# Optimization experiments

Measured on AMD Instinct MI355X. Metric: run time of the kernel, lower is better.

The kernel has to match this reference:

```python
import jax, jax.numpy as jnp
import numpy as np

HEAD_DIM = 64
NUM_Q_HEADS = 32
NUM_KV_HEADS = 8
ROPE_FREQ = 10000.0
EPS = 1e-6


def _rms_norm(x, gamma):
    # normalize over last dim (head_dim)
    var = jnp.mean(jnp.square(x), axis=-1, keepdims=True)
    return x * jax.lax.rsqrt(var + EPS) * gamma


def _rope_cos_sin(seq_len, dtype=jnp.float32):
    inv_freq = 1.0 / (ROPE_FREQ ** (jnp.arange(0, HEAD_DIM, 2, dtype=jnp.float32) / HEAD_DIM))
    pos = jnp.arange(seq_len, dtype=jnp.float32)
    freqs = pos[:, None] * inv_freq[None, :]          # [S, hd/2]
    emb = jnp.concatenate([freqs, freqs], axis=-1)    # [S, hd]
    return jnp.cos(emb).astype(dtype), jnp.sin(emb).astype(dtype)


def _rotate_half(x):
    x1, x2 = jnp.split(x, 2, axis=-1)
    return jnp.concatenate([-x2, x1], axis=-1)


def _apply_rope(x, cos, sin):
    # x: [B, H, S, hd]; cos/sin: [S, hd]
    return x * cos[None, None, :, :] + _rotate_half(x) * sin[None, None, :, :]


def setup_inputs() -> dict:
    key = jax.random.key(0)
    ks = jax.random.split(key, 5)
    B, S, D = 2, 2048, 2048
    qkv_out = (NUM_Q_HEADS + 2 * NUM_KV_HEADS) * HEAD_DIM  # 3072
    x = jax.random.normal(ks[0], (B, S, D), dtype=jnp.float32)
    w_qkv = jax.random.normal(ks[1], (qkv_out, D), dtype=jnp.float32) * (D ** -0.5)
    w_out = jax.random.normal(ks[2], (D, NUM_Q_HEADS * HEAD_DIM), dtype=jnp.float32) * ((NUM_Q_HEADS * HEAD_DIM) ** -0.5)
    q_gamma = jnp.ones((HEAD_DIM,), dtype=jnp.float32)
    k_gamma = jnp.ones((HEAD_DIM,), dtype=jnp.float32)
    return {"x": x, "w_qkv": w_qkv, "w_out": w_out, "q_gamma": q_gamma, "k_gamma": k_gamma}


def reference(x, w_qkv, w_out, q_gamma, k_gamma):
    B, S, D = x.shape
    groups = NUM_Q_HEADS // NUM_KV_HEADS
    # fused QKV projection (no bias)
    qkv = jnp.einsum("bsd,od->bso", x, w_qkv)
    qkv = qkv.reshape(B, S, NUM_Q_HEADS + 2 * NUM_KV_HEADS, HEAD_DIM)
    qkv = jnp.transpose(qkv, (0, 2, 1, 3))  # [B, heads, S, hd]
    q = qkv[:, :NUM_Q_HEADS]
    k = qkv[:, NUM_Q_HEADS:NUM_Q_HEADS + NUM_KV_HEADS]
    v = qkv[:, NUM_Q_HEADS + NUM_KV_HEADS:]
    # QK RMSNorm over head_dim
    q = _rms_norm(q, q_gamma)
    k = _rms_norm(k, k_gamma)
    # RoPE
    cos, sin = _rope_cos_sin(S, dtype=x.dtype)
    q = _apply_rope(q, cos, sin)
    k = _apply_rope(k, cos, sin)
    # GQA: repeat-interleave kv heads
    k = jnp.repeat(k, groups, axis=1)
    v = jnp.repeat(v, groups, axis=1)
    # causal SDPA
    scale = HEAD_DIM ** -0.5
    scores = jnp.einsum("bhqd,bhkd->bhqk", q, k) * scale
    causal = jnp.tril(jnp.ones((S, S), dtype=bool))
    scores = jnp.where(causal[None, None], scores, jnp.finfo(scores.dtype).min)
    attn = jax.nn.softmax(scores, axis=-1)
    ctx = jnp.einsum("bhqk,bhkd->bhqd", attn, v)
    ctx = jnp.transpose(ctx, (0, 2, 1, 3)).reshape(B, S, NUM_Q_HEADS * HEAD_DIM)
    out = jnp.einsum("bsf,df->bsd", ctx, w_out)
    return out
```

## Files before the change

### kernel.cpp

```cpp
#include <hip/hip_runtime.h>

typedef _Float16 f16;
typedef __fp16 fp16x2 __attribute__((ext_vector_type(2)));
typedef _Float16 f16x8 __attribute__((ext_vector_type(8)));
typedef float f32x4 __attribute__((ext_vector_type(4)));
typedef float f32x16 __attribute__((ext_vector_type(16)));

#define AS1 __attribute__((address_space(1)))
#define AS3 __attribute__((address_space(3)))

#define SCALE_L2E 0.18033688011112042f


__device__ __forceinline__ void gload16(const void* g, void* l) {
    __builtin_amdgcn_global_load_lds(
        (const AS1 unsigned*)(unsigned long long)g,
        (AS3 unsigned*)(unsigned)(unsigned long long)l,
        16, 0, 0);
}

__device__ __forceinline__ unsigned pk2(float a, float b) {
    union { fp16x2 v; unsigned u; } c;
    c.v = __builtin_amdgcn_cvt_pkrtz(a, b);
    return c.u;
}

#define BAR() do { asm volatile("" ::: "memory"); __builtin_amdgcn_s_barrier(); asm volatile("" ::: "memory"); } while (0)


__global__ __launch_bounds__(256) void k_cast_all(const float* __restrict__ x,
                                                  const float* __restrict__ wq,
                                                  const float* __restrict__ wo,
                                                  f16* __restrict__ Xh,
                                                  f16* __restrict__ Wqh,
                                                  f16* __restrict__ Woh,
                                                  float* __restrict__ cosT,
                                                  float* __restrict__ sinT) {
    if (blockIdx.x >= 18432) {
        int idx = (blockIdx.x - 18432) * 256 + threadIdx.x;
        int s = idx >> 5, i = idx & 31;
        float ang = (float)s * exp2f(-(float)i * 0.4152410118609190f);
        cosT[idx] = cosf(ang);
        sinT[idx] = sinf(ang);
        return;
    }
    int i = (blockIdx.x * 256 + threadIdx.x) * 4;
    const float* src; f16* dst;
    if (i < 8388608)        { src = x  + i;            dst = Xh  + i; }
    else if (i < 14680064)  { src = wq + (i - 8388608); dst = Wqh + (i - 8388608); }
    else                    { src = wo + (i - 14680064); dst = Woh + (i - 14680064); }
    float4 v = *(const float4*)src;
    union { f16 h[4]; ushort4 u; } c;
    c.h[0] = (f16)v.x; c.h[1] = (f16)v.y; c.h[2] = (f16)v.z; c.h[3] = (f16)v.w;
    *(ushort4*)dst = c.u;
}


template <typename OutT, int NU>
__global__ __launch_bounds__(512, 2) void k_gemm256(const f16* __restrict__ A,
                                                    const f16* __restrict__ Bt,
                                                    OutT* __restrict__ C,
                                                    int M, int N, int K) {
    constexpr int BUFSZ = 32768 + NU * 8192;
    __shared__ __align__(16) char sm[2 * BUFSZ];
    const int tid = threadIdx.x;
    const int lane = tid & 63, wid = tid >> 6;
    const int wm = wid >> 2, wn = wid & 3;
    const int lr = lane & 15, g4 = lane >> 4;

    const int gx = gridDim.x;
    const int nwg = gx * gridDim.y;
    int lin = blockIdx.y * gx + blockIdx.x;
    lin = (lin & 7) * (nwg >> 3) + (lin >> 3);
    const int bx = lin % gx, by = lin / gx;
    const int m0 = by * 256, n0 = bx * (64 * NU);
    const int NT = K >> 6;

    const int srow = tid >> 3;
    const int scol = ((tid & 7) ^ (srow & 7)) * 8;
    const f16* gA = A  + (size_t)(m0 + srow) * K + scol;
    const f16* gB = Bt + (size_t)(n0 + srow) * K + scol;

    auto STGA = [&](int t, int h) {
        char* d = sm + (t & 1) * BUFSZ + h * 16384 + tid * 16;
        gload16(gA + (size_t)(h * 128) * K + t * 64,      d);
        gload16(gA + (size_t)(h * 128 + 64) * K + t * 64, d + 8192);
    };
    auto STGB = [&](int t) {
#pragma unroll
        for (int u = 0; u < NU; u++)
            gload16(gB + (size_t)(u * 64) * K + t * 64,
                    sm + (t & 1) * BUFSZ + 32768 + u * 8192 + tid * 16);
    };

    f32x4 acc[8][NU] = {};
    f16x8 bfr[NU];

    STGA(0, 0); STGA(0, 1); STGB(0);
    STGA(1, 0); STGA(1, 1); STGB(1);
    if constexpr (NU == 2) asm volatile("s_waitcnt vmcnt(6)" ::: "memory");
    else                   asm volatile("s_waitcnt vmcnt(7)" ::: "memory");
    BAR();

    for (int t = 0; t < NT; ++t) {
        const int buf = t & 1;
        const char* bA = sm + buf * BUFSZ + wm * 16384;
        const char* bB = sm + buf * BUFSZ + 32768;
        const bool sA = (t >= 1) && (t + 1 < NT);
        const bool sB = (t + 2 < NT);
#pragma unroll
        for (int p = 0; p < 4; ++p) {
            const int kk = p >> 1, mh = p & 1;
            f16x8 afr[4];
            if (mh == 0) {
#pragma unroll
                for (int n = 0; n < NU; n++) {
                    const int r = wn * (16 * NU) + n * 16 + lr;
                    bfr[n] = *(const f16x8*)(bB + ((r * 128 + kk * 64 + g4 * 16) ^ ((r & 7) << 4)));
                }
            }
#pragma unroll
            for (int i = 0; i < 4; i++) {
                const int r = (mh * 4 + i) * 16 + lr;
                afr[i] = *(const f16x8*)(bA + ((r * 128 + kk * 64 + g4 * 16) ^ ((r & 7) << 4)));
            }
            if (p == 0 && sA) STGA(t + 1, 0);
            if (p == 1 && sA) STGA(t + 1, 1);
            if (p == 3 && sB) STGB(t + 2);
            BAR();
            asm volatile("s_waitcnt lgkmcnt(0)" ::: "memory");
            __builtin_amdgcn_s_setprio(1);
#pragma unroll
            for (int i = 0; i < 4; i++)
#pragma unroll
                for (int n = 0; n < NU; n++)
                    acc[mh * 4 + i][n] = __builtin_amdgcn_mfma_f32_16x16x32_f16(afr[i], bfr[n], acc[mh * 4 + i][n], 0, 0, 0);
            __builtin_amdgcn_s_setprio(0);
            if (p == 3 && t + 1 < NT) {
                if (t + 2 < NT) {
                    if constexpr (NU == 2) asm volatile("s_waitcnt vmcnt(2)" ::: "memory");
                    else                   asm volatile("s_waitcnt vmcnt(3)" ::: "memory");
                } else {
                    asm volatile("s_waitcnt vmcnt(0)" ::: "memory");
                }
            }
            BAR();
        }
    }

#pragma unroll
    for (int m = 0; m < 8; m++)
#pragma unroll
        for (int n = 0; n < NU; n++) {
            size_t base = (size_t)(m0 + wm * 128 + m * 16 + g4 * 4) * N + (n0 + wn * (16 * NU) + n * 16 + lr);
#pragma unroll
            for (int j = 0; j < 4; j++)
                C[base + (size_t)j * N] = (OutT)acc[m][n][j];
        }
}


__global__ __launch_bounds__(256) void k_qkv_post(const f16* __restrict__ qkv,
                                                  const float* __restrict__ qg,
                                                  const float* __restrict__ kg,
                                                  const float* __restrict__ cosT,
                                                  const float* __restrict__ sinT,
                                                  f16* __restrict__ Qf,
                                                  f16* __restrict__ Kf,
                                                  f16* __restrict__ Vf) {
    __shared__ f16 tl[4][8][72];
    const int tid = threadIdx.x, lane = tid & 63, wv = tid >> 6;
    const int gw = blockIdx.x * 4 + wv;
    const int b = gw / 12288;
    const int r0 = gw - b * 12288;
    const int head = r0 >> 8;
    const int sblk = r0 & 255;
    const int s0 = sblk * 8;
    const int s_loc = lane >> 3, ch = lane & 7;
    const int s = s0 + s_loc;

    f16x8 v = *(const f16x8*)&qkv[((size_t)b * 2048 + s) * 3072 + head * 64 + ch * 8];

    if (head < 40) {
        float vf[8];
#pragma unroll
        for (int j = 0; j < 8; j++) vf[j] = (float)v[j];
        float ss = 0.f;
#pragma unroll
        for (int j = 0; j < 8; j++) ss += vf[j] * vf[j];
        ss += __shfl_xor(ss, 1); ss += __shfl_xor(ss, 2); ss += __shfl_xor(ss, 4);
        float rinv = rsqrtf(ss * (1.0f / 64.0f) + 1e-6f);
        const float* gam = (head < 32 ? qg : kg) + ch * 8;
        float4 g0 = *(const float4*)gam, g1 = *(const float4*)(gam + 4);
        float gv[8] = {g0.x, g0.y, g0.z, g0.w, g1.x, g1.y, g1.z, g1.w};
        float xn[8], ot[8];
#pragma unroll
        for (int j = 0; j < 8; j++) xn[j] = vf[j] * rinv * gv[j];
#pragma unroll
        for (int j = 0; j < 8; j++) ot[j] = __shfl_xor(xn[j], 4);
        const int i0 = (ch & 3) * 8;
        float4 c0  = *(const float4*)&cosT[(s << 5) + i0];
        float4 c1  = *(const float4*)&cosT[(s << 5) + i0 + 4];
        float4 sn0 = *(const float4*)&sinT[(s << 5) + i0];
        float4 sn1 = *(const float4*)&sinT[(s << 5) + i0 + 4];
        float cs[8] = {c0.x, c0.y, c0.z, c0.w, c1.x, c1.y, c1.z, c1.w};
        float sn[8] = {sn0.x, sn0.y, sn0.z, sn0.w, sn1.x, sn1.y, sn1.z, sn1.w};
        float sgn = (ch < 4) ? -1.0f : 1.0f;
        float ov[8];
#pragma unroll
        for (int j = 0; j < 8; j++) ov[j] = xn[j] * cs[j] + sgn * ot[j] * sn[j];
        if (head < 32) {
#pragma unroll
            for (int j = 0; j < 8; j++) ov[j] *= SCALE_L2E;
        }
        uint4 o;
        o.x = pk2(ov[0], ov[1]); o.y = pk2(ov[2], ov[3]);
        o.z = pk2(ov[4], ov[5]); o.w = pk2(ov[6], ov[7]);
        const int t = s >> 5;
        const int lane2 = (s & 31) + ((ch & 1) << 5);
        const int c = ch >> 1;
        f16* dst = (head < 32)
            ? Qf + (((size_t)(b * 32 + head) * 256 + t * 4 + c) * 512 + lane2 * 8)
            : Kf + (((size_t)(b * 8 + head - 32) * 256 + t * 4 + c) * 512 + lane2 * 8);
        *(uint4*)dst = o;
    } else {
        const int kh = head - 40;
        *(f16x8*)&tl[wv][s_loc][ch * 8] = v;
        asm volatile("s_waitcnt lgkmcnt(0)" ::: "memory");
        f16x8 cv;
#pragma unroll
        for (int rr = 0; rr < 8; rr++) cv[rr] = tl[wv][rr][lane];
        const int d = lane, dh = d >> 5;
        const int t = s0 >> 5, c = (s0 >> 4) & 1, hv = (s0 >> 3) & 1;
        const int g = dh * 2 + c;
        f16* dst = Vf + (((size_t)(b * 8 + kh) * 256 + t * 4 + g) * 512
                         + ((d & 31) + (hv << 5)) * 8);
        *(f16x8*)dst = cv;
    }
}


struct AttnPart { f32x16 o0, o1; float l; };

__device__ __forceinline__ void do_exp(const f32x16& st, unsigned* X, float& lrun) {
    float ps0 = 0.0f, ps1 = 0.0f;
#pragma unroll
    for (int j = 0; j < 8; j++) {
        float p0 = __builtin_amdgcn_exp2f(st[2 * j]);
        float p1 = __builtin_amdgcn_exp2f(st[2 * j + 1]);
        ps0 += p0; ps1 += p1;
        X[j] = pk2(p0, p1);
    }
    lrun += ps0 + ps1;
}

__device__ __forceinline__ void do_pv(const f16x8* va, const f16x8* vb,
                                      const unsigned* X, f32x16& o0, f32x16& o1) {
#pragma unroll
    for (int c = 0; c < 2; c++) {
        unsigned a0 = X[4 * c], a1 = X[4 * c + 1], a2 = X[4 * c + 2], a3 = X[4 * c + 3];
        asm volatile("v_permlane32_swap_b32 %0, %1" : "+v"(a0), "+v"(a2));
        asm volatile("v_permlane32_swap_b32 %0, %1" : "+v"(a1), "+v"(a3));
        union { unsigned u[4]; f16x8 v; } pb;
        pb.u[0] = a0; pb.u[1] = a1; pb.u[2] = a2; pb.u[3] = a3;
        o0 = __builtin_amdgcn_mfma_f32_32x32x16_f16(va[c], pb.v, o0, 0, 0, 0);
        o1 = __builtin_amdgcn_mfma_f32_32x32x16_f16(vb[c], pb.v, o1, 0, 0, 0);
    }
}

__device__ __forceinline__ void do_mask(f32x16& st, int lq, int hi) {
#pragma unroll
    for (int r = 0; r < 16; r++) {
        int kvl = (r & 3) + ((r >> 2) << 3) + (hi << 2);
        if (kvl > lq) st[r] = -1e30f;
    }
}

__device__ __forceinline__ AttnPart attn_part(int qb, int par, int lane, int lq, int hi,
        const f16* __restrict__ Qfp, const f16* __restrict__ Kfp,
        const f16* __restrict__ Vfp) {
    f16x8 qf[4];
#pragma unroll
    for (int c = 0; c < 4; c++)
        qf[c] = *(const f16x8*)&Qfp[((size_t)qb * 4 + c) * 512 + lane * 8];

    AttnPart P;
    P.o0 = (f32x16){}; P.o1 = (f32x16){};
    float lrun = 0.0f;

    f16x8 kfa[4], kfb[4], vaa[2], vba[2], vab[2], vbb[2];

    auto LOADK = [&](f16x8* kf, int t) {
#pragma unroll
        for (int c = 0; c < 4; c++)
            kf[c] = *(const f16x8*)&Kfp[((size_t)t * 4 + c) * 512 + lane * 8];
    };
    auto LOADV = [&](f16x8* va, f16x8* vb, int t) {
#pragma unroll
        for (int c = 0; c < 2; c++) {
            va[c] = *(const f16x8*)&Vfp[((size_t)t * 4 + c)     * 512 + lane * 8];
            vb[c] = *(const f16x8*)&Vfp[((size_t)t * 4 + 2 + c) * 512 + lane * 8];
        }
    };

    int kt = par;
    if (kt <= qb)     { LOADK(kfa, kt);     LOADV(vaa, vba, kt); }
    if (kt + 2 <= qb) { LOADK(kfb, kt + 2); LOADV(vab, vbb, kt + 2); }

    while (kt + 2 <= qb) {
        const int nx = kt + 4;
        f32x16 sta = {};
#pragma unroll
        for (int c = 0; c < 4; c++)
            sta = __builtin_amdgcn_mfma_f32_32x32x16_f16(kfa[c], qf[c], sta, 0, 0, 0);
        unsigned Xa[8];
        do_exp(sta, Xa, lrun);

        f32x16 stb = {};
#pragma unroll
        for (int c = 0; c < 4; c++)
            stb = __builtin_amdgcn_mfma_f32_32x32x16_f16(kfb[c], qf[c], stb, 0, 0, 0);
        if (nx <= qb) LOADK(kfa, nx);

        do_pv(vaa, vba, Xa, P.o0, P.o1);
        if (nx <= qb) LOADV(vaa, vba, nx);

        if (kt + 2 == qb) do_mask(stb, lq, hi);
        unsigned Xb[8];
        do_exp(stb, Xb, lrun);
        if (nx + 2 <= qb) LOADK(kfb, nx + 2);

        do_pv(vab, vbb, Xb, P.o0, P.o1);
        if (nx + 2 <= qb) LOADV(vab, vbb, nx + 2);

        kt = nx;
    }
    if (kt <= qb) {
        f32x16 st = {};
#pragma unroll
        for (int c = 0; c < 4; c++)
            st = __builtin_amdgcn_mfma_f32_32x32x16_f16(kfa[c], qf[c], st, 0, 0, 0);
        if (kt == qb) do_mask(st, lq, hi);
        unsigned X[8];
        do_exp(st, X, lrun);
        do_pv(vaa, vba, X, P.o0, P.o1);
    }

    P.l = lrun + __shfl_xor(lrun, 32);
    return P;
}

__global__ __launch_bounds__(128) void k_attn(const f16* __restrict__ Qf,
                                              const f16* __restrict__ Kf,
                                              const f16* __restrict__ Vf,
                                              f16* __restrict__ ctx) {
    __shared__ float ldsO[32][65];
    __shared__ float ldsL[32];
    const int tid = threadIdx.x;
    const int par = tid >> 6, lane = tid & 63;
    const int lq = lane & 31, hi = lane >> 5;
    const int bh = blockIdx.y, b = bh >> 5, h = bh & 31, kh = h >> 2;
    const int pj = blockIdx.x;

    const f16* Qfp = Qf + (size_t)(b * 32 + h) * 131072;
    const f16* Kfp = Kf + (size_t)(b * 8 + kh) * 131072;
    const f16* Vfp = Vf + (size_t)(b * 8 + kh) * 131072;
    f16*       ctxbase = ctx + (size_t)b * 2048 * 2048 + h * 64;

    const int qbs[2] = {pj, 63 - pj};
#pragma unroll
    for (int s = 0; s < 2; s++) {
        const int qb = qbs[s];
        AttnPart P = attn_part(qb, par, lane, lq, hi, Qfp, Kfp, Vfp);

        if (par == 1) {
            if (hi == 0) ldsL[lq] = P.l;
#pragma unroll
            for (int r = 0; r < 16; r++) {
                int d = (r & 3) + ((r >> 2) << 3) + (hi << 2);
                ldsO[lq][d]      = P.o0[r];
                ldsO[lq][d + 32] = P.o1[r];
            }
        }
        __syncthreads();
        if (par == 0) {
            float inv = 1.0f / (P.l + ldsL[lq]);
            unsigned* row = (unsigned*)(ctxbase + (size_t)(qb * 32 + lq) * 2048);
#pragma unroll
            for (int g = 0; g < 4; g++) {
                int d = 8 * g + 4 * hi;
                float c0 = (P.o0[4 * g]     + ldsO[lq][d])     * inv;
                float c1 = (P.o0[4 * g + 1] + ldsO[lq][d + 1]) * inv;
                float c2 = (P.o0[4 * g + 2] + ldsO[lq][d + 2]) * inv;
                float c3 = (P.o0[4 * g + 3] + ldsO[lq][d + 3]) * inv;
                uint2 a; a.x = pk2(c0, c1); a.y = pk2(c2, c3);
                *(uint2*)(row + 2 * hi + 4 * g) = a;
                float e0 = (P.o1[4 * g]     + ldsO[lq][d + 32]) * inv;
                float e1 = (P.o1[4 * g + 1] + ldsO[lq][d + 33]) * inv;
                float e2 = (P.o1[4 * g + 2] + ldsO[lq][d + 34]) * inv;
                float e3 = (P.o1[4 * g + 3] + ldsO[lq][d + 35]) * inv;
                uint2 e; e.x = pk2(e0, e1); e.y = pk2(e2, e3);
                *(uint2*)(row + 16 + 2 * hi + 4 * g) = e;
            }
        }
        __syncthreads();
    }
}


extern "C" void kernel_launch(void* const* d_in, const int* in_sizes, int n_in,
                              void* d_out, int out_size, void* d_ws, size_t ws_size,
                              hipStream_t stream) {
    const float* x     = (const float*)d_in[0];
    const float* w_qkv = (const float*)d_in[1];
    const float* w_out = (const float*)d_in[2];
    const float* qg    = (const float*)d_in[3];
    const float* kg    = (const float*)d_in[4];
    float* out = (float*)d_out;
    char* ws = (char*)d_ws;

    float* cosT = (float*)(ws);
    float* sinT = (float*)(ws + 262144);
    f16* Xh     = (f16*)(ws + 524288);
    f16* Wqkvh  = (f16*)(ws + 17301504);
    f16* Wouth  = (f16*)(ws + 29884416);
    f16* QKVh   = (f16*)(ws + 38273024);
    f16* Qfb    = (f16*)(ws + 63438848);
    f16* Kfb    = (f16*)(ws + 80216064);
    f16* Vfb    = (f16*)(ws + 84410368);
    f16* Ctxh   = (f16*)(ws + 88604672);

    k_cast_all<<<18688, 256, 0, stream>>>(x, w_qkv, w_out, Xh, Wqkvh, Wouth, cosT, sinT);

    k_gemm256<f16, 3><<<dim3(16, 16), 512, 0, stream>>>(Xh, Wqkvh, QKVh, 4096, 3072, 2048);

    k_qkv_post<<<6144, 256, 0, stream>>>(QKVh, qg, kg, cosT, sinT, Qfb, Kfb, Vfb);

    k_attn<<<dim3(32, 64), 128, 0, stream>>>(Qfb, Kfb, Vfb, Ctxh);

    k_gemm256<float, 2><<<dim3(16, 16), 512, 0, stream>>>(Ctxh, Wouth, out, 4096, 2048, 2048);
}
```

Baseline: 187.1 us.

## Share K/V tiles across four query blocks via LDS double buffering in attention

The attention kernel changes from two waves splitting each query block's KV range to four waves that each own one of four adjacent query blocks. K/V tiles are staged once per block into double-buffered LDS with global_load_lds and read by all four waves, which cuts redundant global K/V traffic. The cross-wave partial-sum reduction through LDS goes away. In exchange there are two barriers per KV tile, waves whose causal range has ended sit idle while others finish, and the grid shrinks to 512 blocks with 256 threads each.

```diff
diff --git a/kernel.cpp b/kernel.cpp
--- a/kernel.cpp
+++ b/kernel.cpp
@@ -240,170 +240,115 @@
 }
 
 
-struct AttnPart { f32x16 o0, o1; float l; };
-
-__device__ __forceinline__ void do_exp(const f32x16& st, unsigned* X, float& lrun) {
-    float ps0 = 0.0f, ps1 = 0.0f;
-#pragma unroll
-    for (int j = 0; j < 8; j++) {
-        float p0 = __builtin_amdgcn_exp2f(st[2 * j]);
-        float p1 = __builtin_amdgcn_exp2f(st[2 * j + 1]);
-        ps0 += p0; ps1 += p1;
-        X[j] = pk2(p0, p1);
-    }
-    lrun += ps0 + ps1;
-}
-
-__device__ __forceinline__ void do_pv(const f16x8* va, const f16x8* vb,
-                                      const unsigned* X, f32x16& o0, f32x16& o1) {
-#pragma unroll
-    for (int c = 0; c < 2; c++) {
-        unsigned a0 = X[4 * c], a1 = X[4 * c + 1], a2 = X[4 * c + 2], a3 = X[4 * c + 3];
-        asm volatile("v_permlane32_swap_b32 %0, %1" : "+v"(a0), "+v"(a2));
-        asm volatile("v_permlane32_swap_b32 %0, %1" : "+v"(a1), "+v"(a3));
-        union { unsigned u[4]; f16x8 v; } pb;
-        pb.u[0] = a0; pb.u[1] = a1; pb.u[2] = a2; pb.u[3] = a3;
-        o0 = __builtin_amdgcn_mfma_f32_32x32x16_f16(va[c], pb.v, o0, 0, 0, 0);
-        o1 = __builtin_amdgcn_mfma_f32_32x32x16_f16(vb[c], pb.v, o1, 0, 0, 0);
-    }
-}
-
-__device__ __forceinline__ void do_mask(f32x16& st, int lq, int hi) {
-#pragma unroll
-    for (int r = 0; r < 16; r++) {
-        int kvl = (r & 3) + ((r >> 2) << 3) + (hi << 2);
-        if (kvl > lq) st[r] = -1e30f;
-    }
-}
-
-__device__ __forceinline__ AttnPart attn_part(int qb, int par, int lane, int lq, int hi,
-        const f16* __restrict__ Qfp, const f16* __restrict__ Kfp,
-        const f16* __restrict__ Vfp) {
-    f16x8 qf[4];
-#pragma unroll
-    for (int c = 0; c < 4; c++)
-        qf[c] = *(const f16x8*)&Qfp[((size_t)qb * 4 + c) * 512 + lane * 8];
-
-    AttnPart P;
-    P.o0 = (f32x16){}; P.o1 = (f32x16){};
-    float lrun = 0.0f;
-
-    f16x8 kfa[4], kfb[4], vaa[2], vba[2], vab[2], vbb[2];
-
-    auto LOADK = [&](f16x8* kf, int t) {
-#pragma unroll
-        for (int c = 0; c < 4; c++)
-            kf[c] = *(const f16x8*)&Kfp[((size_t)t * 4 + c) * 512 + lane * 8];
-    };
-    auto LOADV = [&](f16x8* va, f16x8* vb, int t) {
-#pragma unroll
-        for (int c = 0; c < 2; c++) {
-            va[c] = *(const f16x8*)&Vfp[((size_t)t * 4 + c)     * 512 + lane * 8];
-            vb[c] = *(const f16x8*)&Vfp[((size_t)t * 4 + 2 + c) * 512 + lane * 8];
-        }
-    };
-
-    int kt = par;
-    if (kt <= qb)     { LOADK(kfa, kt);     LOADV(vaa, vba, kt); }
-    if (kt + 2 <= qb) { LOADK(kfb, kt + 2); LOADV(vab, vbb, kt + 2); }
-
-    while (kt + 2 <= qb) {
-        const int nx = kt + 4;
-        f32x16 sta = {};
-#pragma unroll
-        for (int c = 0; c < 4; c++)
-            sta = __builtin_amdgcn_mfma_f32_32x32x16_f16(kfa[c], qf[c], sta, 0, 0, 0);
-        unsigned Xa[8];
-        do_exp(sta, Xa, lrun);
-
-        f32x16 stb = {};
-#pragma unroll
-        for (int c = 0; c < 4; c++)
-            stb = __builtin_amdgcn_mfma_f32_32x32x16_f16(kfb[c], qf[c], stb, 0, 0, 0);
-        if (nx <= qb) LOADK(kfa, nx);
-
-        do_pv(vaa, vba, Xa, P.o0, P.o1);
-        if (nx <= qb) LOADV(vaa, vba, nx);
-
-        if (kt + 2 == qb) do_mask(stb, lq, hi);
-        unsigned Xb[8];
-        do_exp(stb, Xb, lrun);
-        if (nx + 2 <= qb) LOADK(kfb, nx + 2);
-
-        do_pv(vab, vbb, Xb, P.o0, P.o1);
-        if (nx + 2 <= qb) LOADV(vab, vbb, nx + 2);
-
-        kt = nx;
-    }
-    if (kt <= qb) {
-        f32x16 st = {};
-#pragma unroll
-        for (int c = 0; c < 4; c++)
-            st = __builtin_amdgcn_mfma_f32_32x32x16_f16(kfa[c], qf[c], st, 0, 0, 0);
-        if (kt == qb) do_mask(st, lq, hi);
-        unsigned X[8];
-        do_exp(st, X, lrun);
-        do_pv(vaa, vba, X, P.o0, P.o1);
-    }
-
-    P.l = lrun + __shfl_xor(lrun, 32);
-    return P;
-}
-
-__global__ __launch_bounds__(128) void k_attn(const f16* __restrict__ Qf,
+__global__ __launch_bounds__(256) void k_attn(const f16* __restrict__ Qf,
                                               const f16* __restrict__ Kf,
                                               const f16* __restrict__ Vf,
                                               f16* __restrict__ ctx) {
-    __shared__ float ldsO[32][65];
-    __shared__ float ldsL[32];
-    const int tid = threadIdx.x;
-    const int par = tid >> 6, lane = tid & 63;
+    __shared__ __align__(16) char kv[2][8192];
+    const int tid = threadIdx.x, lane = tid & 63, w = tid >> 6;
     const int lq = lane & 31, hi = lane >> 5;
     const int bh = blockIdx.y, b = bh >> 5, h = bh & 31, kh = h >> 2;
-    const int pj = blockIdx.x;
 
     const f16* Qfp = Qf + (size_t)(b * 32 + h) * 131072;
     const f16* Kfp = Kf + (size_t)(b * 8 + kh) * 131072;
     const f16* Vfp = Vf + (size_t)(b * 8 + kh) * 131072;
     f16*       ctxbase = ctx + (size_t)b * 2048 * 2048 + h * 64;
 
-    const int qbs[2] = {pj, 63 - pj};
 #pragma unroll
     for (int s = 0; s < 2; s++) {
-        const int qb = qbs[s];
-        AttnPart P = attn_part(qb, par, lane, lq, hi, Qfp, Kfp, Vfp);
-
-        if (par == 1) {
-            if (hi == 0) ldsL[lq] = P.l;
-#pragma unroll
-            for (int r = 0; r < 16; r++) {
-                int d = (r & 3) + ((r >> 2) << 3) + (hi << 2);
-                ldsO[lq][d]      = P.o0[r];
-                ldsO[lq][d + 32] = P.o1[r];
-            }
-        }
-        __syncthreads();
-        if (par == 0) {
-            float inv = 1.0f / (P.l + ldsL[lq]);
-            unsigned* row = (unsigned*)(ctxbase + (size_t)(qb * 32 + lq) * 2048);
-#pragma unroll
-            for (int g = 0; g < 4; g++) {
-                int d = 8 * g + 4 * hi;
-                float c0 = (P.o0[4 * g]     + ldsO[lq][d])     * inv;
-                float c1 = (P.o0[4 * g + 1] + ldsO[lq][d + 1]) * inv;
-                float c2 = (P.o0[4 * g + 2] + ldsO[lq][d + 2]) * inv;
-                float c3 = (P.o0[4 * g + 3] + ldsO[lq][d + 3]) * inv;
-                uint2 a; a.x = pk2(c0, c1); a.y = pk2(c2, c3);
-                *(uint2*)(row + 2 * hi + 4 * g) = a;
-                float e0 = (P.o1[4 * g]     + ldsO[lq][d + 32]) * inv;
-                float e1 = (P.o1[4 * g + 1] + ldsO[lq][d + 33]) * inv;
-                float e2 = (P.o1[4 * g + 2] + ldsO[lq][d + 34]) * inv;
-                float e3 = (P.o1[4 * g + 3] + ldsO[lq][d + 35]) * inv;
-                uint2 e; e.x = pk2(e0, e1); e.y = pk2(e2, e3);
-                *(uint2*)(row + 16 + 2 * hi + 4 * g) = e;
-            }
-        }
-        __syncthreads();
+        const int g  = s == 0 ? (int)blockIdx.x : 15 - (int)blockIdx.x;
+        const int qb = g * 4 + w;
+        const int nt = g * 4 + 4;
+
+        f16x8 qf[4];
+#pragma unroll
+        for (int c = 0; c < 4; c++)
+            qf[c] = *(const f16x8*)&Qfp[((size_t)qb * 4 + c) * 512 + lane * 8];
+
+        f32x16 o0 = {}, o1 = {};
+        float lrun = 0.0f;
+
+        auto STAGE = [&](int t) {
+            gload16(Kfp + (size_t)t * 2048 + tid * 8, kv[t & 1] + tid * 16);
+            gload16(Vfp + (size_t)t * 2048 + tid * 8, kv[t & 1] + 4096 + tid * 16);
+        };
+
+        STAGE(0); STAGE(1);
+        asm volatile("s_waitcnt vmcnt(2)" ::: "memory");
+        BAR();
+
+        for (int t = 0; t < nt; ++t) {
+            const char* bufp = kv[t & 1];
+            if (t <= qb) {
+                f16x8 kfr[4];
+#pragma unroll
+                for (int c = 0; c < 4; c++)
+                    kfr[c] = *(const f16x8*)(bufp + c * 1024 + lane * 16);
+                f32x16 st = {};
+#pragma unroll
+                for (int c = 0; c < 4; c++)
+                    st = __builtin_amdgcn_mfma_f32_32x32x16_f16(kfr[c], qf[c], st, 0, 0, 0);
+
+                f16x8 va[2], vb[2];
+#pragma unroll
+                for (int c = 0; c < 2; c++) {
+                    va[c] = *(const f16x8*)(bufp + 4096 + c * 1024 + lane * 16);
+                    vb[c] = *(const f16x8*)(bufp + 4096 + (2 + c) * 1024 + lane * 16);
+                }
+
+                if (t == qb) {
+#pragma unroll
+                    for (int r = 0; r < 16; r++) {
+                        int kvl = (r & 3) + ((r >> 2) << 3) + (hi << 2);
+                        if (kvl > lq) st[r] = -1e30f;
+                    }
+                }
+
+                unsigned X[8];
+                float ps0 = 0.0f, ps1 = 0.0f;
+#pragma unroll
+                for (int j = 0; j < 8; j++) {
+                    float p0 = __builtin_amdgcn_exp2f(st[2 * j]);
+                    float p1 = __builtin_amdgcn_exp2f(st[2 * j + 1]);
+                    ps0 += p0; ps1 += p1;
+                    X[j] = pk2(p0, p1);
+                }
+                lrun += ps0 + ps1;
+
+#pragma unroll
+                for (int c = 0; c < 2; c++) {
+                    unsigned a0 = X[4 * c], a1 = X[4 * c + 1], a2 = X[4 * c + 2], a3 = X[4 * c + 3];
+                    asm volatile("v_permlane32_swap_b32 %0, %1" : "+v"(a0), "+v"(a2));
+                    asm volatile("v_permlane32_swap_b32 %0, %1" : "+v"(a1), "+v"(a3));
+                    union { unsigned u[4]; f16x8 v; } pb;
+                    pb.u[0] = a0; pb.u[1] = a1; pb.u[2] = a2; pb.u[3] = a3;
+                    o0 = __builtin_amdgcn_mfma_f32_32x32x16_f16(va[c], pb.v, o0, 0, 0, 0);
+                    o1 = __builtin_amdgcn_mfma_f32_32x32x16_f16(vb[c], pb.v, o1, 0, 0, 0);
+                }
+            }
+            BAR();
+            if (t + 2 < nt) {
+                STAGE(t + 2);
+                asm volatile("s_waitcnt vmcnt(2)" ::: "memory");
+            } else if (t + 1 < nt) {
+                asm volatile("s_waitcnt vmcnt(0)" ::: "memory");
+            }
+            BAR();
+        }
+
+        float lt  = lrun + __shfl_xor(lrun, 32);
+        float inv = 1.0f / lt;
+        unsigned* row = (unsigned*)(ctxbase + (size_t)(qb * 32 + lq) * 2048);
+#pragma unroll
+        for (int gg = 0; gg < 4; gg++) {
+            uint2 a, e;
+            a.x = pk2(o0[4 * gg]     * inv, o0[4 * gg + 1] * inv);
+            a.y = pk2(o0[4 * gg + 2] * inv, o0[4 * gg + 3] * inv);
+            *(uint2*)(row + 2 * hi + 4 * gg) = a;
+            e.x = pk2(o1[4 * gg]     * inv, o1[4 * gg + 1] * inv);
+            e.y = pk2(o1[4 * gg + 2] * inv, o1[4 * gg + 3] * inv);
+            *(uint2*)(row + 16 + 2 * hi + 4 * gg) = e;
+        }
     }
 }
 
@@ -436,7 +381,7 @@
 
     k_qkv_post<<<6144, 256, 0, stream>>>(QKVh, qg, kg, cosT, sinT, Qfb, Kfb, Vfb);
 
-    k_attn<<<dim3(32, 64), 128, 0, stream>>>(Qfb, Kfb, Vfb, Ctxh);
+    k_attn<<<dim3(8, 64), 256, 0, stream>>>(Qfb, Kfb, Vfb, Ctxh);
 
     k_gemm256<float, 2><<<dim3(16, 16), 512, 0, stream>>>(Ctxh, Wouth, out, 4096, 2048, 2048);
 }
```

Result: no change. 189.5 us (+1.3%).
